# Performance work log

Hardware: AMD Instinct MI355X
Metric: run time of the kernel (lower is better)

## Reference

```python
import jax, jax.numpy as jnp
import numpy as np

D_MODEL = 512
N_HEADS = 8
B, L = 4, 2048


def setup_inputs() -> dict:
    key = jax.random.key(0)
    ks = jax.random.split(key, 7)
    s = 1.0 / np.sqrt(D_MODEL)
    return {
        "queries": jax.random.normal(ks[0], (B, L, 3, D_MODEL), jnp.float32),
        "keys": jax.random.normal(ks[1], (B, L, 3, D_MODEL), jnp.float32),
        "values": jax.random.normal(ks[2], (B, L, 3, D_MODEL), jnp.float32),
        "Wq": jax.random.normal(ks[3], (D_MODEL, D_MODEL), jnp.float32) * s,
        "Wk": jax.random.normal(ks[4], (D_MODEL, D_MODEL), jnp.float32) * s,
        "Wv": jax.random.normal(ks[5], (D_MODEL, D_MODEL), jnp.float32) * s,
        "Wo": jax.random.normal(ks[6], (D_MODEL, D_MODEL), jnp.float32) * s,
    }


def _vn_linear(x, W):
    # VNLinear: bias-free linear over the channel (last) dim, acting per vector component.
    # x: [B, L, 3, Din], W: [Dout, Din] (torch nn.Linear convention: y = x @ W^T)
    return jnp.einsum('blvc,dc->blvd', x, W)


def reference(queries, keys, values, Wq, Wk, Wv, Wo):
    Bq, Lq, _, _ = queries.shape
    H = N_HEADS
    q = _vn_linear(queries, Wq).reshape(Bq, Lq, 3, H, -1)   # [B,L,3,H,E]
    k = _vn_linear(keys, Wk).reshape(Bq, Lq, 3, H, -1)
    v = _vn_linear(values, Wv).reshape(Bq, Lq, 3, H, -1)
    E = q.shape[-1]
    scale = 1.0 / np.sqrt(E)
    # score contracts both the vector (v=3) and head-dim axes
    score = jnp.einsum('blvhd,bsvhd->bhls', q, k)            # [B,H,L,S]
    attn = jax.nn.softmax(scale * score, axis=-1)
    V = jnp.einsum('bhls,bsvhd->blvhd', attn, v)             # [B,L,3,H,E]
    out = V.reshape(Bq, Lq, 3, -1)                            # [B,L,3,D]
    out = _vn_linear(out, Wo)
    return out, attn
```

## Files before the change

kernel.cpp:

```cpp
#include <hip/hip_runtime.h>
#include <hip/hip_bf16.h>

typedef __attribute__((ext_vector_type(8))) short  bf16x8s;
typedef __attribute__((ext_vector_type(4))) float  f32x4;

#define MFMA_BF(a,b,c) __builtin_amdgcn_mfma_f32_16x16x32_bf16(a,b,c,0,0,0)

__device__ __forceinline__ unsigned short f2bf(float f){
  unsigned int u = __builtin_bit_cast(unsigned int, f);
  u += 0x7FFFu + ((u >> 16) & 1u);
  return (unsigned short)(u >> 16);
}
__device__ __forceinline__ float bf2f(unsigned short h){
  return __builtin_bit_cast(float, (unsigned int)h << 16);
}

#define LL   2048
#define DD   512
#define HH   8
#define CC   192
#define OUT0 12582912
#define L3V  6144
#define SCL  0.18033688011112042f

#define QH_OFF   0u
#define KH_OFF   25165824u
#define VT_OFF   50331648u
#define OH_OFF   75497472u
#define WB_OFF   100663296u
#define RINV_OFF 102760448u
#define WS_NEEDED 103022592u

__global__ __launch_bounds__(256) void k_prep_w(
    const float* __restrict__ Wq, const float* __restrict__ Wk,
    const float* __restrict__ Wv, const float* __restrict__ Wo,
    unsigned short* __restrict__ Wb)
{
  int i = blockIdx.x*256 + threadIdx.x;
  Wb[i]           = f2bf(Wq[i]*SCL);
  Wb[262144 + i]  = f2bf(Wk[i]);
  Wb[524288 + i]  = f2bf(Wv[i]);
  Wb[786432 + i]  = f2bf(Wo[i]);
}

__global__ __launch_bounds__(256, 3) void k_proj_qkv(
    const float* __restrict__ xq, const float* __restrict__ xk, const float* __restrict__ xv,
    const unsigned short* __restrict__ Wb,
    unsigned short* __restrict__ Qh, unsigned short* __restrict__ Kh,
    unsigned short* __restrict__ Vt)
{
  const int t = blockIdx.z;
  const float* __restrict__ x = (t==0) ? xq : ((t==1) ? xk : xv);
  const unsigned short* __restrict__ W = Wb + t*262144;
  const int rowBase = blockIdx.x*64;
  const int nBase   = blockIdx.y*256;
  const int tid = threadIdx.x, w = tid>>6, l = tid&63, g = l>>4, li = l&15;

  __shared__ unsigned short Wlds[256*40];
  __shared__ unsigned short Tl[64*65];

  const int arow = rowBase + w*16 + li;
  const float* __restrict__ xrow = x + (size_t)arow*DD;

  f32x4 acc[16];
  #pragma unroll
  for (int nt = 0; nt < 16; ++nt) acc[nt] = (f32x4){0,0,0,0};

  bf16x8s wreg[4];
  #pragma unroll
  for (int i = 0; i < 4; ++i){
    const int f = i*256 + tid, r = f>>2, c8 = f&3;
    wreg[i] = *(const bf16x8s*)(W + (size_t)(nBase + r)*DD + c8*8);
  }
  float4 xa = *(const float4*)(xrow + g*8);
  float4 xb = *(const float4*)(xrow + g*8 + 4);

  for (int kk = 0; kk < 16; ++kk){
    __syncthreads();
    #pragma unroll
    for (int i = 0; i < 4; ++i){
      const int f = i*256 + tid, r = f>>2, c8 = f&3;
      *(bf16x8s*)(Wlds + r*40 + c8*8) = wreg[i];
    }
    __syncthreads();

    bf16x8s a;
    a[0]=(short)f2bf(xa.x); a[1]=(short)f2bf(xa.y); a[2]=(short)f2bf(xa.z); a[3]=(short)f2bf(xa.w);
    a[4]=(short)f2bf(xb.x); a[5]=(short)f2bf(xb.y); a[6]=(short)f2bf(xb.z); a[7]=(short)f2bf(xb.w);

    if (kk < 15){
      const int k0n = (kk+1)*32;
      #pragma unroll
      for (int i = 0; i < 4; ++i){
        const int f = i*256 + tid, r = f>>2, c8 = f&3;
        wreg[i] = *(const bf16x8s*)(W + (size_t)(nBase + r)*DD + k0n + c8*8);
      }
      xa = *(const float4*)(xrow + k0n + g*8);
      xb = *(const float4*)(xrow + k0n + g*8 + 4);
    }

    __builtin_amdgcn_s_setprio(1);
    #pragma unroll
    for (int nt = 0; nt < 16; ++nt){
      bf16x8s b = *(const bf16x8s*)(Wlds + (nt*16 + li)*40 + g*8);
      acc[nt] = MFMA_BF(a, b, acc[nt]);
    }
    __builtin_amdgcn_s_setprio(0);
  }

  if (t == 2){
    const int b    = rowBase / L3V;
    const int rloc = rowBase - b*L3V;
    for (int hb = 0; hb < 4; ++hb){
      __syncthreads();
      #pragma unroll
      for (int nt2 = 0; nt2 < 4; ++nt2)
        #pragma unroll
        for (int j = 0; j < 4; ++j)
          Tl[(w*16 + g*4 + j)*65 + nt2*16 + li] = f2bf(acc[hb*4 + nt2][j]);
      __syncthreads();
      if (tid < 192){
        const int v = tid >> 6, e = tid & 63;
        const int ls0 = (rloc - v + 2)/3;
        const int ls1 = (rloc + 63 - v)/3;
        const int hg  = (nBase >> 6) + hb;
        unsigned short* __restrict__ dst = Vt + ((size_t)((b*HH + hg)*CC + v*64 + e))*LL;
        for (int ls = ls0; ls <= ls1; ++ls){
          const int ml = 3*ls + v - rloc;
          dst[ls] = Tl[ml*65 + e];
        }
      }
    }
  } else {
    unsigned short* __restrict__ P = (t==0) ? Qh : Kh;
    #pragma unroll
    for (int nt = 0; nt < 16; ++nt){
      #pragma unroll
      for (int j = 0; j < 4; ++j){
        const int m  = rowBase + w*16 + g*4 + j;
        const int d  = nBase + nt*16 + li;
        const int b  = m / L3V;
        const int rm = m - b*L3V;
        const int ls = rm / 3;
        const int v  = rm - ls*3;
        const int h  = d >> 6, e = d & 63;
        P[((size_t)(b*HH + h)*LL + ls)*CC + v*64 + e] = f2bf(acc[nt][j]);
      }
    }
  }
}

__global__ __launch_bounds__(256, 2) void k_attn(
    const unsigned short* __restrict__ Qh, const unsigned short* __restrict__ Kh,
    const unsigned short* __restrict__ Vt,
    float* __restrict__ attnp, unsigned short* __restrict__ Oh,
    float* __restrict__ rinvArr)
{
  const int bid  = blockIdx.x;
  const int xcd  = bid & 7, slot = bid >> 3;
  const int bh   = xcd*4 + (slot >> 5);
  const int qt   = slot & 31;
  const int tid = threadIdx.x, w = tid>>6, l = tid&63, g = l>>4, li = l&15;

  const unsigned short* __restrict__ Q = Qh + (size_t)bh*LL*CC;
  const unsigned short* __restrict__ K = Kh + (size_t)bh*LL*CC;
  const unsigned short* __restrict__ V = Vt + (size_t)bh*CC*LL;
  unsigned short* __restrict__ A16 =
      (unsigned short*)(attnp + (size_t)bh*LL*LL + (size_t)(qt*64)*LL);

  __shared__ unsigned short Klds[64*200];
  __shared__ unsigned short Vlds[192*72];
  __shared__ unsigned short Plds[64*72];

  bf16x8s aq[6];
  const unsigned short* __restrict__ qrow = Q + (size_t)(qt*64 + w*16 + li)*CC;
  #pragma unroll
  for (int ks = 0; ks < 6; ++ks) aq[ks] = *(const bf16x8s*)(qrow + ks*32 + g*8);

  f32x4 oacc[12];
  #pragma unroll
  for (int ct = 0; ct < 12; ++ct) oacc[ct] = (f32x4){0,0,0,0};
  float ssum[4] = {0.f,0.f,0.f,0.f};

  bf16x8s kreg[6], vreg[6];
  #pragma unroll
  for (int i = 0; i < 6; ++i){
    const int f = i*256 + tid;
    kreg[i] = *(const bf16x8s*)(K + (size_t)f*8);
    vreg[i] = *(const bf16x8s*)(V + (size_t)(f>>3)*LL + (f&7)*8);
  }

  for (int st = 0; st < 32; ++st){
    __syncthreads();
    #pragma unroll
    for (int i = 0; i < 6; ++i){
      const int f  = i*256 + tid;
      const int kr = f / 24, ksg = f - kr*24;
      *(bf16x8s*)(Klds + kr*200 + ksg*8)       = kreg[i];
      *(bf16x8s*)(Vlds + (f>>3)*72 + (f&7)*8)  = vreg[i];
    }
    __syncthreads();
    if (st < 31){
      #pragma unroll
      for (int i = 0; i < 6; ++i){
        const int f = i*256 + tid;
        kreg[i] = *(const bf16x8s*)(K + (size_t)(st+1)*12288 + (size_t)f*8);
        vreg[i] = *(const bf16x8s*)(V + (size_t)(f>>3)*LL + (st+1)*64 + (f&7)*8);
      }
    }

    f32x4 sc[4] = { {0,0,0,0},{0,0,0,0},{0,0,0,0},{0,0,0,0} };
    __builtin_amdgcn_s_setprio(1);
    #pragma unroll
    for (int ks = 0; ks < 6; ++ks){
      #pragma unroll
      for (int nt = 0; nt < 4; ++nt){
        bf16x8s b = *(const bf16x8s*)(Klds + (nt*16 + li)*200 + ks*32 + g*8);
        sc[nt] = MFMA_BF(aq[ks], b, sc[nt]);
      }
    }
    __builtin_amdgcn_s_setprio(0);

    #pragma unroll
    for (int nt = 0; nt < 4; ++nt){
      #pragma unroll
      for (int j = 0; j < 4; ++j){
        float p = exp2f(sc[nt][j] - 8.0f);
        ssum[j] += p;
        Plds[(w*16 + g*4 + j)*72 + nt*16 + li] = f2bf(p);
      }
    }

    __builtin_amdgcn_s_setprio(1);
    #pragma unroll
    for (int kkk = 0; kkk < 2; ++kkk){
      bf16x8s pa = *(const bf16x8s*)(Plds + (w*16 + li)*72 + kkk*32 + g*8);
      #pragma unroll
      for (int ct = 0; ct < 12; ++ct){
        bf16x8s bv = *(const bf16x8s*)(Vlds + (ct*16 + li)*72 + kkk*32 + g*8);
        oacc[ct] = MFMA_BF(pa, bv, oacc[ct]);
      }
    }
    __builtin_amdgcn_s_setprio(0);

    #pragma unroll
    for (int u = 0; u < 2; ++u){
      const int c  = u*64 + l;
      const int r  = c >> 3;
      const int c8 = c & 7;
      bf16x8s pv = *(const bf16x8s*)(Plds + (w*16 + r)*72 + c8*8);
      *(bf16x8s*)(A16 + (size_t)(w*16 + r)*4096 + st*64 + c8*8) = pv;
    }
  }

  float rinv[4];
  #pragma unroll
  for (int j = 0; j < 4; ++j){
    float s = ssum[j];
    s += __shfl_xor(s, 1); s += __shfl_xor(s, 2);
    s += __shfl_xor(s, 4); s += __shfl_xor(s, 8);
    rinv[j] = 1.0f / s;
  }
  if (li == 0){
    #pragma unroll
    for (int j = 0; j < 4; ++j)
      rinvArr[bh*LL + qt*64 + w*16 + g*4 + j] = rinv[j];
  }
  #pragma unroll
  for (int ct = 0; ct < 12; ++ct){
    #pragma unroll
    for (int j = 0; j < 4; ++j){
      const int row = qt*64 + w*16 + g*4 + j;
      Oh[((size_t)bh*LL + row)*CC + ct*16 + li] = f2bf(oacc[ct][j] * rinv[j]);
    }
  }
}

__global__ __launch_bounds__(256) void k_scale_attn(
    float* __restrict__ attnp, const float* __restrict__ rinvArr)
{
  const int row = blockIdx.x;
  const float r = rinvArr[row];
  float* __restrict__ rowp = attnp + (size_t)row*LL;
  const unsigned short* __restrict__ p16 = (const unsigned short*)rowp;

  bf16x8s v = *(const bf16x8s*)(p16 + threadIdx.x*8);
  __syncthreads();

  f32x4 o0, o1;
  o0[0] = bf2f((unsigned short)v[0])*r; o0[1] = bf2f((unsigned short)v[1])*r;
  o0[2] = bf2f((unsigned short)v[2])*r; o0[3] = bf2f((unsigned short)v[3])*r;
  o1[0] = bf2f((unsigned short)v[4])*r; o1[1] = bf2f((unsigned short)v[5])*r;
  o1[2] = bf2f((unsigned short)v[6])*r; o1[3] = bf2f((unsigned short)v[7])*r;
  f32x4* __restrict__ dst = (f32x4*)(rowp + threadIdx.x*8);
  __builtin_nontemporal_store(o0, dst);
  __builtin_nontemporal_store(o1, dst + 1);
}

__global__ __launch_bounds__(256, 3) void k_proj_out(
    const unsigned short* __restrict__ Oh, const unsigned short* __restrict__ Wo,
    float* __restrict__ out)
{
  const int rowBase = blockIdx.x*64;
  const int nBase   = blockIdx.y*256;
  const int tid = threadIdx.x, w = tid>>6, l = tid&63, g = l>>4, li = l&15;

  __shared__ unsigned short Wlds[256*40];

  const int m  = rowBase + w*16 + li;
  const int b  = m / L3V;
  const int rm = m - b*L3V;
  const int ls = rm / 3;
  const int v  = rm - ls*3;
  const unsigned short* __restrict__ obase = Oh + ((size_t)(b*HH)*LL + ls)*CC + v*64;

  f32x4 acc[16];
  #pragma unroll
  for (int nt = 0; nt < 16; ++nt) acc[nt] = (f32x4){0,0,0,0};

  bf16x8s wreg[4];
  #pragma unroll
  for (int i = 0; i < 4; ++i){
    const int f = i*256 + tid, r = f>>2, c8 = f&3;
    wreg[i] = *(const bf16x8s*)(Wo + (size_t)(nBase + r)*DD + c8*8);
  }
  bf16x8s acur = *(const bf16x8s*)(obase + g*8);

  for (int kk = 0; kk < 16; ++kk){
    __syncthreads();
    #pragma unroll
    for (int i = 0; i < 4; ++i){
      const int f = i*256 + tid, r = f>>2, c8 = f&3;
      *(bf16x8s*)(Wlds + r*40 + c8*8) = wreg[i];
    }
    __syncthreads();

    bf16x8s a = acur;
    if (kk < 15){
      const int kn = kk + 1;
      const int k0n = kn*32;
      acur = *(const bf16x8s*)(obase + (size_t)(kn>>1)*(LL*CC) + (kn&1)*32 + g*8);
      #pragma unroll
      for (int i = 0; i < 4; ++i){
        const int f = i*256 + tid, r = f>>2, c8 = f&3;
        wreg[i] = *(const bf16x8s*)(Wo + (size_t)(nBase + r)*DD + k0n + c8*8);
      }
    }

    __builtin_amdgcn_s_setprio(1);
    #pragma unroll
    for (int nt = 0; nt < 16; ++nt){
      bf16x8s bfr = *(const bf16x8s*)(Wlds + (nt*16 + li)*40 + g*8);
      acc[nt] = MFMA_BF(a, bfr, acc[nt]);
    }
    __builtin_amdgcn_s_setprio(0);
  }

  #pragma unroll
  for (int nt = 0; nt < 16; ++nt){
    #pragma unroll
    for (int j = 0; j < 4; ++j){
      const int mr = rowBase + w*16 + g*4 + j;
      out[(size_t)mr*DD + nBase + nt*16 + li] = acc[nt][j];
    }
  }
}

extern "C" void kernel_launch(void* const* d_in, const int* in_sizes, int n_in,
                              void* d_out, int out_size, void* d_ws, size_t ws_size,
                              hipStream_t stream)
{
  const float* xq = (const float*)d_in[0];
  const float* xk = (const float*)d_in[1];
  const float* xv = (const float*)d_in[2];
  const float* Wq = (const float*)d_in[3];
  const float* Wk = (const float*)d_in[4];
  const float* Wv = (const float*)d_in[5];
  const float* Wo = (const float*)d_in[6];

  if (ws_size < (size_t)WS_NEEDED) return;

  float* out  = (float*)d_out;
  float* attn = out + OUT0;

  char* ws = (char*)d_ws;
  unsigned short* Qh = (unsigned short*)(ws + QH_OFF);
  unsigned short* Kh = (unsigned short*)(ws + KH_OFF);
  unsigned short* Vt = (unsigned short*)(ws + VT_OFF);
  unsigned short* Oh = (unsigned short*)(ws + OH_OFF);
  unsigned short* Wb = (unsigned short*)(ws + WB_OFF);
  float*        rinv = (float*)(ws + RINV_OFF);

  hipLaunchKernelGGL(k_prep_w,    dim3(1024),      dim3(256), 0, stream, Wq, Wk, Wv, Wo, Wb);
  hipLaunchKernelGGL(k_proj_qkv,  dim3(384, 2, 3), dim3(256), 0, stream, xq, xk, xv, Wb, Qh, Kh, Vt);
  hipLaunchKernelGGL(k_attn,      dim3(1024),      dim3(256), 0, stream, Qh, Kh, Vt, attn, Oh, rinv);
  hipLaunchKernelGGL(k_scale_attn,dim3(65536),     dim3(256), 0, stream, attn, rinv);
  hipLaunchKernelGGL(k_proj_out,  dim3(384, 2),    dim3(256), 0, stream, Oh, Wb + 786432, out);
}
```

Before: 497.5 us.

## Double attention block rows to share K/V tiles and fuse tail kernels

The attention kernel now runs 512 threads covering 128 query rows per block, so each K/V tile staged in shared memory serves twice as many rows. The P buffer is split per half-block. The output projection and the attention-rescale pass are merged into one launch, with blocks dispatched by index, which removes a kernel boundary and lets the two overlap. The price is a larger block and a launch bound of (512,4) that forces tighter register limits, which could cause spills given the 12 output accumulators plus the Q fragments.

```diff
diff --git a/kernel.cpp b/kernel.cpp
--- a/kernel.cpp
+++ b/kernel.cpp
@@ -150,7 +150,7 @@
   }
 }
 
-__global__ __launch_bounds__(256, 2) void k_attn(
+__global__ __launch_bounds__(512, 4) void k_attn(
     const unsigned short* __restrict__ Qh, const unsigned short* __restrict__ Kh,
     const unsigned short* __restrict__ Vt,
     float* __restrict__ attnp, unsigned short* __restrict__ Oh,
@@ -158,22 +158,23 @@
 {
   const int bid  = blockIdx.x;
   const int xcd  = bid & 7, slot = bid >> 3;
-  const int bh   = xcd*4 + (slot >> 5);
-  const int qt   = slot & 31;
+  const int bh   = xcd*4 + (slot >> 4);
+  const int qt   = slot & 15;
   const int tid = threadIdx.x, w = tid>>6, l = tid&63, g = l>>4, li = l&15;
+  const int ph = w >> 2, wr = (w & 3)*16;
 
   const unsigned short* __restrict__ Q = Qh + (size_t)bh*LL*CC;
   const unsigned short* __restrict__ K = Kh + (size_t)bh*LL*CC;
   const unsigned short* __restrict__ V = Vt + (size_t)bh*CC*LL;
   unsigned short* __restrict__ A16 =
-      (unsigned short*)(attnp + (size_t)bh*LL*LL + (size_t)(qt*64)*LL);
+      (unsigned short*)(attnp + (size_t)bh*LL*LL + (size_t)(qt*128)*LL);
 
   __shared__ unsigned short Klds[64*200];
   __shared__ unsigned short Vlds[192*72];
-  __shared__ unsigned short Plds[64*72];
+  __shared__ unsigned short Plds[2][64*72];
 
   bf16x8s aq[6];
-  const unsigned short* __restrict__ qrow = Q + (size_t)(qt*64 + w*16 + li)*CC;
+  const unsigned short* __restrict__ qrow = Q + (size_t)(qt*128 + w*16 + li)*CC;
   #pragma unroll
   for (int ks = 0; ks < 6; ++ks) aq[ks] = *(const bf16x8s*)(qrow + ks*32 + g*8);
 
@@ -182,10 +183,10 @@
   for (int ct = 0; ct < 12; ++ct) oacc[ct] = (f32x4){0,0,0,0};
   float ssum[4] = {0.f,0.f,0.f,0.f};
 
-  bf16x8s kreg[6], vreg[6];
-  #pragma unroll
-  for (int i = 0; i < 6; ++i){
-    const int f = i*256 + tid;
+  bf16x8s kreg[3], vreg[3];
+  #pragma unroll
+  for (int i = 0; i < 3; ++i){
+    const int f = i*512 + tid;
     kreg[i] = *(const bf16x8s*)(K + (size_t)f*8);
     vreg[i] = *(const bf16x8s*)(V + (size_t)(f>>3)*LL + (f&7)*8);
   }
@@ -193,8 +194,8 @@
   for (int st = 0; st < 32; ++st){
     __syncthreads();
     #pragma unroll
-    for (int i = 0; i < 6; ++i){
-      const int f  = i*256 + tid;
+    for (int i = 0; i < 3; ++i){
+      const int f  = i*512 + tid;
       const int kr = f / 24, ksg = f - kr*24;
       *(bf16x8s*)(Klds + kr*200 + ksg*8)       = kreg[i];
       *(bf16x8s*)(Vlds + (f>>3)*72 + (f&7)*8)  = vreg[i];
@@ -202,8 +203,8 @@
     __syncthreads();
     if (st < 31){
       #pragma unroll
-      for (int i = 0; i < 6; ++i){
-        const int f = i*256 + tid;
+      for (int i = 0; i < 3; ++i){
+        const int f = i*512 + tid;
         kreg[i] = *(const bf16x8s*)(K + (size_t)(st+1)*12288 + (size_t)f*8);
         vreg[i] = *(const bf16x8s*)(V + (size_t)(f>>3)*LL + (st+1)*64 + (f&7)*8);
       }
@@ -227,14 +228,14 @@
       for (int j = 0; j < 4; ++j){
         float p = exp2f(sc[nt][j] - 8.0f);
         ssum[j] += p;
-        Plds[(w*16 + g*4 + j)*72 + nt*16 + li] = f2bf(p);
+        Plds[ph][(wr + g*4 + j)*72 + nt*16 + li] = f2bf(p);
       }
     }
 
     __builtin_amdgcn_s_setprio(1);
     #pragma unroll
     for (int kkk = 0; kkk < 2; ++kkk){
-      bf16x8s pa = *(const bf16x8s*)(Plds + (w*16 + li)*72 + kkk*32 + g*8);
+      bf16x8s pa = *(const bf16x8s*)(Plds[ph] + (wr + li)*72 + kkk*32 + g*8);
       #pragma unroll
       for (int ct = 0; ct < 12; ++ct){
         bf16x8s bv = *(const bf16x8s*)(Vlds + (ct*16 + li)*72 + kkk*32 + g*8);
@@ -248,7 +249,7 @@
       const int c  = u*64 + l;
       const int r  = c >> 3;
       const int c8 = c & 7;
-      bf16x8s pv = *(const bf16x8s*)(Plds + (w*16 + r)*72 + c8*8);
+      bf16x8s pv = *(const bf16x8s*)(Plds[ph] + (wr + r)*72 + c8*8);
       *(bf16x8s*)(A16 + (size_t)(w*16 + r)*4096 + st*64 + c8*8) = pv;
     }
   }
@@ -264,105 +265,106 @@
   if (li == 0){
     #pragma unroll
     for (int j = 0; j < 4; ++j)
-      rinvArr[bh*LL + qt*64 + w*16 + g*4 + j] = rinv[j];
+      rinvArr[bh*LL + qt*128 + w*16 + g*4 + j] = rinv[j];
   }
   #pragma unroll
   for (int ct = 0; ct < 12; ++ct){
     #pragma unroll
     for (int j = 0; j < 4; ++j){
-      const int row = qt*64 + w*16 + g*4 + j;
+      const int row = qt*128 + w*16 + g*4 + j;
       Oh[((size_t)bh*LL + row)*CC + ct*16 + li] = f2bf(oacc[ct][j] * rinv[j]);
     }
   }
 }
 
-__global__ __launch_bounds__(256) void k_scale_attn(
+__global__ __launch_bounds__(256, 3) void k_tail(
+    const unsigned short* __restrict__ Oh, const unsigned short* __restrict__ Wo,
+    float* __restrict__ out,
     float* __restrict__ attnp, const float* __restrict__ rinvArr)
 {
-  const int row = blockIdx.x;
-  const float r = rinvArr[row];
-  float* __restrict__ rowp = attnp + (size_t)row*LL;
-  const unsigned short* __restrict__ p16 = (const unsigned short*)rowp;
-
-  bf16x8s v = *(const bf16x8s*)(p16 + threadIdx.x*8);
-  __syncthreads();
-
-  f32x4 o0, o1;
-  o0[0] = bf2f((unsigned short)v[0])*r; o0[1] = bf2f((unsigned short)v[1])*r;
-  o0[2] = bf2f((unsigned short)v[2])*r; o0[3] = bf2f((unsigned short)v[3])*r;
-  o1[0] = bf2f((unsigned short)v[4])*r; o1[1] = bf2f((unsigned short)v[5])*r;
-  o1[2] = bf2f((unsigned short)v[6])*r; o1[3] = bf2f((unsigned short)v[7])*r;
-  f32x4* __restrict__ dst = (f32x4*)(rowp + threadIdx.x*8);
-  __builtin_nontemporal_store(o0, dst);
-  __builtin_nontemporal_store(o1, dst + 1);
-}
-
-__global__ __launch_bounds__(256, 3) void k_proj_out(
-    const unsigned short* __restrict__ Oh, const unsigned short* __restrict__ Wo,
-    float* __restrict__ out)
-{
-  const int rowBase = blockIdx.x*64;
-  const int nBase   = blockIdx.y*256;
-  const int tid = threadIdx.x, w = tid>>6, l = tid&63, g = l>>4, li = l&15;
-
   __shared__ unsigned short Wlds[256*40];
-
-  const int m  = rowBase + w*16 + li;
-  const int b  = m / L3V;
-  const int rm = m - b*L3V;
-  const int ls = rm / 3;
-  const int v  = rm - ls*3;
-  const unsigned short* __restrict__ obase = Oh + ((size_t)(b*HH)*LL + ls)*CC + v*64;
-
-  f32x4 acc[16];
-  #pragma unroll
-  for (int nt = 0; nt < 16; ++nt) acc[nt] = (f32x4){0,0,0,0};
-
-  bf16x8s wreg[4];
-  #pragma unroll
-  for (int i = 0; i < 4; ++i){
-    const int f = i*256 + tid, r = f>>2, c8 = f&3;
-    wreg[i] = *(const bf16x8s*)(Wo + (size_t)(nBase + r)*DD + c8*8);
-  }
-  bf16x8s acur = *(const bf16x8s*)(obase + g*8);
-
-  for (int kk = 0; kk < 16; ++kk){
-    __syncthreads();
+  const int bid = blockIdx.x;
+  const int tid = threadIdx.x;
+
+  if (bid < 768){
+    const int rowBase = (bid >> 1)*64;
+    const int nBase   = (bid & 1)*256;
+    const int w = tid>>6, l = tid&63, g = l>>4, li = l&15;
+
+    const int m  = rowBase + w*16 + li;
+    const int b  = m / L3V;
+    const int rm = m - b*L3V;
+    const int ls = rm / 3;
+    const int v  = rm - ls*3;
+    const unsigned short* __restrict__ obase = Oh + ((size_t)(b*HH)*LL + ls)*CC + v*64;
+
+    f32x4 acc[16];
+    #pragma unroll
+    for (int nt = 0; nt < 16; ++nt) acc[nt] = (f32x4){0,0,0,0};
+
+    bf16x8s wreg[4];
     #pragma unroll
     for (int i = 0; i < 4; ++i){
       const int f = i*256 + tid, r = f>>2, c8 = f&3;
-      *(bf16x8s*)(Wlds + r*40 + c8*8) = wreg[i];
-    }
-    __syncthreads();
-
-    bf16x8s a = acur;
-    if (kk < 15){
-      const int kn = kk + 1;
-      const int k0n = kn*32;
-      acur = *(const bf16x8s*)(obase + (size_t)(kn>>1)*(LL*CC) + (kn&1)*32 + g*8);
+      wreg[i] = *(const bf16x8s*)(Wo + (size_t)(nBase + r)*DD + c8*8);
+    }
+    bf16x8s acur = *(const bf16x8s*)(obase + g*8);
+
+    for (int kk = 0; kk < 16; ++kk){
+      __syncthreads();
       #pragma unroll
       for (int i = 0; i < 4; ++i){
         const int f = i*256 + tid, r = f>>2, c8 = f&3;
-        wreg[i] = *(const bf16x8s*)(Wo + (size_t)(nBase + r)*DD + k0n + c8*8);
-      }
-    }
-
-    __builtin_amdgcn_s_setprio(1);
+        *(bf16x8s*)(Wlds + r*40 + c8*8) = wreg[i];
+      }
+      __syncthreads();
+
+      bf16x8s a = acur;
+      if (kk < 15){
+        const int kn = kk + 1;
+        const int k0n = kn*32;
+        acur = *(const bf16x8s*)(obase + (size_t)(kn>>1)*(LL*CC) + (kn&1)*32 + g*8);
+        #pragma unroll
+        for (int i = 0; i < 4; ++i){
+          const int f = i*256 + tid, r = f>>2, c8 = f&3;
+          wreg[i] = *(const bf16x8s*)(Wo + (size_t)(nBase + r)*DD + k0n + c8*8);
+        }
+      }
+
+      __builtin_amdgcn_s_setprio(1);
+      #pragma unroll
+      for (int nt = 0; nt < 16; ++nt){
+        bf16x8s bfr = *(const bf16x8s*)(Wlds + (nt*16 + li)*40 + g*8);
+        acc[nt] = MFMA_BF(a, bfr, acc[nt]);
+      }
+      __builtin_amdgcn_s_setprio(0);
+    }
+
     #pragma unroll
     for (int nt = 0; nt < 16; ++nt){
-      bf16x8s bfr = *(const bf16x8s*)(Wlds + (nt*16 + li)*40 + g*8);
-      acc[nt] = MFMA_BF(a, bfr, acc[nt]);
-    }
-    __builtin_amdgcn_s_setprio(0);
-  }
-
-  #pragma unroll
-  for (int nt = 0; nt < 16; ++nt){
-    #pragma unroll
-    for (int j = 0; j < 4; ++j){
-      const int mr = rowBase + w*16 + g*4 + j;
-      out[(size_t)mr*DD + nBase + nt*16 + li] = acc[nt][j];
-    }
+      #pragma unroll
+      for (int j = 0; j < 4; ++j){
+        const int mr = rowBase + w*16 + g*4 + j;
+        out[(size_t)mr*DD + nBase + nt*16 + li] = acc[nt][j];
+      }
+    }
+  } else {
+    const int row = bid - 768;
+    const float r = rinvArr[row];
+    float* __restrict__ rowp = attnp + (size_t)row*LL;
+    const unsigned short* __restrict__ p16 = (const unsigned short*)rowp;
+
+    bf16x8s v = *(const bf16x8s*)(p16 + tid*8);
+    __syncthreads();
+
+    f32x4 o0, o1;
+    o0[0] = bf2f((unsigned short)v[0])*r; o0[1] = bf2f((unsigned short)v[1])*r;
+    o0[2] = bf2f((unsigned short)v[2])*r; o0[3] = bf2f((unsigned short)v[3])*r;
+    o1[0] = bf2f((unsigned short)v[4])*r; o1[1] = bf2f((unsigned short)v[5])*r;
+    o1[2] = bf2f((unsigned short)v[6])*r; o1[3] = bf2f((unsigned short)v[7])*r;
+    f32x4* __restrict__ dst = (f32x4*)(rowp + tid*8);
+    __builtin_nontemporal_store(o0, dst);
+    __builtin_nontemporal_store(o1, dst + 1);
   }
 }
 
@@ -391,9 +393,8 @@
   unsigned short* Wb = (unsigned short*)(ws + WB_OFF);
   float*        rinv = (float*)(ws + RINV_OFF);
 
-  hipLaunchKernelGGL(k_prep_w,    dim3(1024),      dim3(256), 0, stream, Wq, Wk, Wv, Wo, Wb);
-  hipLaunchKernelGGL(k_proj_qkv,  dim3(384, 2, 3), dim3(256), 0, stream, xq, xk, xv, Wb, Qh, Kh, Vt);
-  hipLaunchKernelGGL(k_attn,      dim3(1024),      dim3(256), 0, stream, Qh, Kh, Vt, attn, Oh, rinv);
-  hipLaunchKernelGGL(k_scale_attn,dim3(65536),     dim3(256), 0, stream, attn, rinv);
-  hipLaunchKernelGGL(k_proj_out,  dim3(384, 2),    dim3(256), 0, stream, Oh, Wb + 786432, out);
-}
+  hipLaunchKernelGGL(k_prep_w,   dim3(1024),      dim3(256), 0, stream, Wq, Wk, Wv, Wo, Wb);
+  hipLaunchKernelGGL(k_proj_qkv, dim3(384, 2, 3), dim3(256), 0, stream, xq, xk, xv, Wb, Qh, Kh, Vt);
+  hipLaunchKernelGGL(k_attn,     dim3(512),       dim3(512), 0, stream, Qh, Kh, Vt, attn, Oh, rinv);
+  hipLaunchKernelGGL(k_tail,     dim3(66304),     dim3(256), 0, stream, Oh, Wb + 786432, out, attn, rinv);
+}
```

Measured after the change: 572.5 us. 15.1% more time.
